# Performance work log

Measured on AMD Instinct MI355X. Metric: run time of the kernel, lower is better.

The kernel has to match this reference:

```python
import jax, jax.numpy as jnp
import numpy as np

B, N, DIM = 16, 1024, 512
H, DH = 8, 64
INNER = H * DH            # 512
FF = 4 * DIM              # 2048
CIN = 2 * DIM             # conv inner dim = dim*expansion_factor = 1024
K = 31                    # depthwise kernel size
MAXPOS = 512
EPS = 1e-5


def layernorm(x, g, b):
    mu = jnp.mean(x, axis=-1, keepdims=True)
    var = jnp.mean(jnp.square(x - mu), axis=-1, keepdims=True)
    return (x - mu) * jax.lax.rsqrt(var + EPS) * g + b


def swish(x):
    return x * jax.nn.sigmoid(x)


def feed_forward(x, w1, b1, w2, b2):
    h = swish(x @ w1 + b1)
    return h @ w2 + b2


def setup_inputs() -> dict:
    key = jax.random.key(0)
    ks = jax.random.split(key, 16)
    s = 0.02
    w = lambda k, shape: (jax.random.normal(k, shape, jnp.float32) * s)
    inp = {
        "x": jax.random.normal(ks[0], (B, N, DIM), jnp.float32),
        # FF1
        "ff1_ln_g": jnp.ones((DIM,), jnp.float32), "ff1_ln_b": jnp.zeros((DIM,), jnp.float32),
        "ff1_w1": w(ks[1], (DIM, FF)), "ff1_b1": jnp.zeros((FF,), jnp.float32),
        "ff1_w2": w(ks[2], (FF, DIM)), "ff1_b2": jnp.zeros((DIM,), jnp.float32),
        # Attention (PreNorm)
        "attn_ln_g": jnp.ones((DIM,), jnp.float32), "attn_ln_b": jnp.zeros((DIM,), jnp.float32),
        "wq": w(ks[3], (DIM, INNER)),
        "wkv": w(ks[4], (DIM, 2 * INNER)),
        "wo": w(ks[5], (INNER, DIM)), "bo": jnp.zeros((DIM,), jnp.float32),
        "rel_emb": w(ks[6], (2 * MAXPOS + 1, DH)),
        # Conv module
        "conv_ln_g": jnp.ones((DIM,), jnp.float32), "conv_ln_b": jnp.zeros((DIM,), jnp.float32),
        "conv1_w": w(ks[7], (DIM, 2 * CIN)), "conv1_b": jnp.zeros((2 * CIN,), jnp.float32),
        "dw_w": w(ks[8], (CIN, 1, K)), "dw_b": jnp.zeros((CIN,), jnp.float32),
        "conv2_w": w(ks[9], (CIN, DIM)), "conv2_b": jnp.zeros((DIM,), jnp.float32),
        # FF2
        "ff2_ln_g": jnp.ones((DIM,), jnp.float32), "ff2_ln_b": jnp.zeros((DIM,), jnp.float32),
        "ff2_w1": w(ks[10], (DIM, FF)), "ff2_b1": jnp.zeros((FF,), jnp.float32),
        "ff2_w2": w(ks[11], (FF, DIM)), "ff2_b2": jnp.zeros((DIM,), jnp.float32),
        # post norm
        "post_ln_g": jnp.ones((DIM,), jnp.float32), "post_ln_b": jnp.zeros((DIM,), jnp.float32),
    }
    return inp


def attention(x, wq, wkv, wo, bo, rel_emb):
    b, n, _ = x.shape
    scale = DH ** -0.5
    q = (x @ wq).reshape(b, n, H, DH).transpose(0, 2, 1, 3)   # b h n d
    kv = x @ wkv
    k = kv[..., :INNER].reshape(b, n, H, DH).transpose(0, 2, 1, 3)
    v = kv[..., INNER:].reshape(b, n, H, DH).transpose(0, 2, 1, 3)
    dots = jnp.einsum("bhid,bhjd->bhij", q, k) * scale
    # relative positional bias via embedding lookup
    seq = jnp.arange(n)
    dist = jnp.clip(seq[:, None] - seq[None, :], -MAXPOS, MAXPOS) + MAXPOS  # [n, n]
    rel = jnp.take(rel_emb, dist, axis=0)                      # [n, n, d]
    pos = jnp.einsum("bhnd,njd->bhnj", q, rel) * scale
    attn = jax.nn.softmax(dots + pos, axis=-1)
    out = jnp.einsum("bhij,bhjd->bhid", attn, v)
    out = out.transpose(0, 2, 1, 3).reshape(b, n, INNER)
    return out @ wo + bo


def conv_module(x, ln_g, ln_b, conv1_w, conv1_b, dw_w, dw_b, conv2_w, conv2_b):
    h = layernorm(x, ln_g, ln_b)                               # [b, n, dim]
    h = h @ conv1_w + conv1_b                                  # pointwise conv -> [b, n, 2*CIN]
    a, g = h[..., :CIN], h[..., CIN:]
    h = a * jax.nn.sigmoid(g)                                  # GLU (channel dim)
    hc = h.transpose(0, 2, 1)                                  # [b, CIN, n]
    hc = jnp.pad(hc, ((0, 0), (0, 0), (K - 1, 0)))             # causal left pad
    hc = jax.lax.conv_general_dilated(
        hc, dw_w, window_strides=(1,), padding="VALID",
        feature_group_count=CIN, dimension_numbers=("NCH", "OIH", "NCH"),
    ) + dw_b[None, :, None]
    h = hc.transpose(0, 2, 1)                                  # [b, n, CIN]
    h = swish(h)
    return h @ conv2_w + conv2_b


def reference(x, ff1_ln_g, ff1_ln_b, ff1_w1, ff1_b1, ff1_w2, ff1_b2,
              attn_ln_g, attn_ln_b, wq, wkv, wo, bo, rel_emb,
              conv_ln_g, conv_ln_b, conv1_w, conv1_b, dw_w, dw_b, conv2_w, conv2_b,
              ff2_ln_g, ff2_ln_b, ff2_w1, ff2_b1, ff2_w2, ff2_b2,
              post_ln_g, post_ln_b):
    x = 0.5 * feed_forward(layernorm(x, ff1_ln_g, ff1_ln_b), ff1_w1, ff1_b1, ff1_w2, ff1_b2) + x
    x = attention(layernorm(x, attn_ln_g, attn_ln_b), wq, wkv, wo, bo, rel_emb) + x
    x = conv_module(x, conv_ln_g, conv_ln_b, conv1_w, conv1_b, dw_w, dw_b, conv2_w, conv2_b) + x
    x = 0.5 * feed_forward(layernorm(x, ff2_ln_g, ff2_ln_b), ff2_w1, ff2_b1, ff2_w2, ff2_b2) + x
    return layernorm(x, post_ln_g, post_ln_b)
```

## Files before the change

### kernel.cpp

```cpp
#include <hip/hip_runtime.h>


#define BN 16384

typedef unsigned short u16;
typedef __attribute__((ext_vector_type(8))) __bf16 bf16x8;
typedef __attribute__((ext_vector_type(4))) float f32x4;
typedef __attribute__((ext_vector_type(8))) unsigned short u16x8;

__device__ __forceinline__ float sigf(float x) { return 1.f / (1.f + __expf(-x)); }
__device__ __forceinline__ u16 f2bf(float f) {
  unsigned int u = __float_as_uint(f);
  u += 0x7FFF + ((u >> 16) & 1);
  return (u16)(u >> 16);
}
__device__ __forceinline__ float bf2f(u16 u) {
  return __uint_as_float(((unsigned int)u) << 16);
}
__device__ __forceinline__ void gl_lds16(const void* g, void* lds) {
  __builtin_amdgcn_global_load_lds(
      (const __attribute__((address_space(1))) unsigned int*)g,
      (__attribute__((address_space(3))) unsigned int*)lds, 16, 0, 0);
}

__global__ __launch_bounds__(256) void ln_kernel(const float* __restrict__ in,
    const float* __restrict__ g, const float* __restrict__ b,
    u16* outb, float* outf) {
  const int row = blockIdx.x;
  const int t = threadIdx.x;
  const float2 v = ((const float2*)(in + (size_t)row * 512))[t];
  float s = v.x + v.y;
  float sq = v.x * v.x + v.y * v.y;
#pragma unroll
  for (int o = 32; o > 0; o >>= 1) {
    s += __shfl_down(s, o);
    sq += __shfl_down(sq, o);
  }
  __shared__ float ss[4], ssq[4];
  if ((t & 63) == 0) { ss[t >> 6] = s; ssq[t >> 6] = sq; }
  __syncthreads();
  s = ss[0] + ss[1] + ss[2] + ss[3];
  sq = ssq[0] + ssq[1] + ssq[2] + ssq[3];
  const float mu = s * (1.f / 512.f);
  const float var = fmaxf(sq * (1.f / 512.f) - mu * mu, 0.f);
  const float rstd = rsqrtf(var + 1e-5f);
  const float2 gg = ((const float2*)g)[t];
  const float2 bb = ((const float2*)b)[t];
  float ox = (v.x - mu) * rstd * gg.x + bb.x;
  float oy = (v.y - mu) * rstd * gg.y + bb.y;
  if (outf) {
    float2 o2 = {ox, oy};
    ((float2*)(outf + (size_t)row * 512))[t] = o2;
  } else {
    ushort2 u2 = {f2bf(ox), f2bf(oy)};
    ((ushort2*)(outb + (size_t)row * 512))[t] = u2;
  }
}

__global__ __launch_bounds__(256) void wtrans(const float* __restrict__ W,
                                              u16* __restrict__ WT, int K, int N) {
  const int n0 = blockIdx.x * 32, k0 = blockIdx.y * 32;
  const int t = threadIdx.x;
  const int tx = t & 31, ty = t >> 5;
  __shared__ float T[32][33];
#pragma unroll
  for (int i = 0; i < 4; ++i)
    T[tx][ty + 8 * i] = W[(size_t)(k0 + ty + 8 * i) * N + n0 + tx];
  __syncthreads();
#pragma unroll
  for (int i = 0; i < 4; ++i)
    WT[(size_t)(n0 + ty + 8 * i) * K + k0 + tx] = f2bf(T[ty + 8 * i][tx]);
}

__global__ __launch_bounds__(256) void cvt_bf16(const float* __restrict__ in,
                                                u16* __restrict__ out, int n) {
  const int i = blockIdx.x * 256 + threadIdx.x;
  if (i < n) out[i] = f2bf(in[i]);
}

__global__ __launch_bounds__(256) void gemm_bf16(const u16* __restrict__ A,
    const u16* __restrict__ WT, const float* __restrict__ bias,
    const float* res, float* Cf, u16* Cb, u16* VTout, int K, int N, int ldc,
    float alpha, int act, int qn, int vt0) {
  __shared__ __align__(16) u16 Ast[128 * 64];
  __shared__ __align__(16) u16 Bst[128 * 64];
  const int t = threadIdx.x;
  int bx = blockIdx.x, by = blockIdx.y;
  {
    const int nx = gridDim.x;
    const int lin = bx + nx * by;
    const int xcd = lin & 7;
    const int s = lin >> 3;
    const int ny8 = gridDim.y >> 3;
    const int sy = s / nx;
    by = xcd * ny8 + sy;
    bx = s - sy * nx;
  }
  const int n0 = bx * 128;
  const int m0 = by * 128;
  const int w = t >> 6;
  const int lc = t & 15, lq = (t >> 4) & 3;
  const int wy = w >> 1, wx = w & 1;
  f32x4 acc[4][4];
#pragma unroll
  for (int i = 0; i < 4; ++i)
#pragma unroll
    for (int j = 0; j < 4; ++j)
#pragma unroll
      for (int r = 0; r < 4; ++r) acc[i][j][r] = 0.f;

  const int koff0 = (lq ^ (lc & 7)) * 8;
  const int koff1 = ((4 + lq) ^ (lc & 7)) * 8;

  for (int kt = 0; kt < K; kt += 64) {
#pragma unroll
    for (int s = 0; s < 4; ++s) {
      const int f = t + 256 * s;
      const int fr = f >> 3;
      const int fc = (f & 7) ^ (fr & 7);
      gl_lds16(&A[(size_t)(m0 + fr) * K + kt + fc * 8], &Ast[f * 8]);
      gl_lds16(&WT[(size_t)(n0 + fr) * K + kt + fc * 8], &Bst[f * 8]);
    }
    __syncthreads();
#pragma unroll
    for (int kk = 0; kk < 2; ++kk) {
      const int koff = kk ? koff1 : koff0;
      bf16x8 bfr[4];
#pragma unroll
      for (int j = 0; j < 4; ++j)
        bfr[j] = *(const bf16x8*)&Bst[(wx * 64 + j * 16 + lc) * 64 + koff];
#pragma unroll
      for (int i = 0; i < 4; ++i) {
        const bf16x8 af = *(const bf16x8*)&Ast[(wy * 64 + i * 16 + lc) * 64 + koff];
#pragma unroll
        for (int j = 0; j < 4; ++j)
          acc[i][j] = __builtin_amdgcn_mfma_f32_16x16x32_bf16(af, bfr[j], acc[i][j], 0, 0, 0);
      }
    }
    __syncthreads();
  }

#pragma unroll
  for (int j = 0; j < 4; ++j) {
    const int col = n0 + wx * 64 + j * 16 + lc;
    const float bj = bias ? bias[col] : 0.f;
    const float al = (col < qn) ? alpha : 1.f;
    const bool vtc = (VTout != nullptr) && (col >= vt0);
#pragma unroll
    for (int i = 0; i < 4; ++i) {
      const int row0 = m0 + wy * 64 + i * 16 + lq * 4;
      float v4[4];
#pragma unroll
      for (int r = 0; r < 4; ++r) {
        float v = acc[i][j][r] + bj;
        if (act) v = v * sigf(v);
        v *= al;
        if (res) v += res[(size_t)(row0 + r) * ldc + col];
        v4[r] = v;
      }
      if (vtc) {
        const int cm = col - vt0;
        const int hh = cm >> 6, dd = cm & 63;
        const int bb = row0 >> 10, nl = row0 & 1023;
        ushort4 o4 = {f2bf(v4[0]), f2bf(v4[1]), f2bf(v4[2]), f2bf(v4[3])};
        *(ushort4*)&VTout[((size_t)((bb * 8 + hh) * 64 + dd)) * 1024 + nl] = o4;
      } else {
#pragma unroll
        for (int r = 0; r < 4; ++r) {
          const size_t off = (size_t)(row0 + r) * ldc + col;
          if (Cf) Cf[off] = v4[r];
          else Cb[off] = f2bf(v4[r]);
        }
      }
    }
  }
}

__global__ __launch_bounds__(256) void attn_mfma(const u16* __restrict__ QKV,
    const u16* __restrict__ Vt, const u16* __restrict__ Rb, u16* __restrict__ O) {
  const int lin = blockIdx.x;
  const int hb = lin & 127;
  const int n0 = (lin >> 7) * 64;
  const int h = hb & 7, b = hb >> 3;
  const int t = threadIdx.x;
  const int w = t >> 6;
  const int lc = t & 15, lq = (t >> 4) & 3;

  __shared__ __align__(16) u16 Ks[2][64 * 64];
  __shared__ __align__(16) u16 Vs[2][64 * 64];
  __shared__ __align__(16) u16 SP[64 * 72];

  bf16x8 qf[2];
  {
    const size_t qrow = (size_t)(b * 1024 + n0 + w * 16 + lc) * 1536 + h * 64;
    qf[0] = *(const bf16x8*)&QKV[qrow + lq * 8];
    qf[1] = *(const bf16x8*)&QKV[qrow + 32 + lq * 8];
  }

  const u16* Kg = QKV + (size_t)b * 1024 * 1536 + 512 + h * 64;
  const u16* Vg = Vt + (size_t)(b * 8 + h) * 64 * 1024;

  const int srow = t >> 3;
  const int scb0 = ((t & 7) ^ (srow & 7)) * 8;
  const int srow1 = (t + 256) >> 3;
  const int scb1 = (((t + 256) & 7) ^ (srow1 & 7)) * 8;

  gl_lds16(&Kg[(size_t)srow * 1536 + scb0], &Ks[0][t * 8]);
  gl_lds16(&Vg[(size_t)srow * 1024 + scb0], &Vs[0][t * 8]);
  gl_lds16(&Kg[(size_t)srow1 * 1536 + scb1], &Ks[0][(t + 256) * 8]);
  gl_lds16(&Vg[(size_t)srow1 * 1024 + scb1], &Vs[0][(t + 256) * 8]);

  float l_r[4] = {0.f, 0.f, 0.f, 0.f};
  f32x4 o[4];
#pragma unroll
  for (int dt = 0; dt < 4; ++dt)
#pragma unroll
    for (int r = 0; r < 4; ++r) o[dt][r] = 0.f;

  const int swz0 = (lq ^ (lc & 7)) * 8;
  const int swz1 = ((4 + lq) ^ (lc & 7)) * 8;

  int buf = 0;
  for (int jt = 0; jt < 16; ++jt) {
    const int j0 = jt * 64;
    __syncthreads();

    if (jt < 15) {
      const int j1 = j0 + 64;
      gl_lds16(&Kg[(size_t)(j1 + srow) * 1536 + scb0], &Ks[buf ^ 1][t * 8]);
      gl_lds16(&Vg[(size_t)srow * 1024 + j1 + scb0], &Vs[buf ^ 1][t * 8]);
      gl_lds16(&Kg[(size_t)(j1 + srow1) * 1536 + scb1], &Ks[buf ^ 1][(t + 256) * 8]);
      gl_lds16(&Vg[(size_t)srow1 * 1024 + j1 + scb1], &Vs[buf ^ 1][(t + 256) * 8]);
    }

    f32x4 qk[4], pa[5];
#pragma unroll
    for (int j = 0; j < 4; ++j)
#pragma unroll
      for (int r = 0; r < 4; ++r) qk[j][r] = 0.f;
#pragma unroll
    for (int rtl = 0; rtl < 5; ++rtl)
#pragma unroll
      for (int r = 0; r < 4; ++r) pa[rtl][r] = 0.f;

    const int base = n0 - j0 - 63;
    const u16* rp[5];
#pragma unroll
    for (int rtl = 0; rtl < 5; ++rtl) {
      int p = base + (w + rtl) * 16 + lc;
      p = (p < -512 ? -512 : (p > 512 ? 512 : p)) + 512;
      rp[rtl] = Rb + (size_t)p * 64 + lq * 8;
    }

#pragma unroll
    for (int ks = 0; ks < 2; ++ks) {
      const int koff = ks ? swz1 : swz0;
      bf16x8 rfr[5];
#pragma unroll
      for (int rtl = 0; rtl < 5; ++rtl)
        rfr[rtl] = *(const bf16x8*)&rp[rtl][ks * 32];
#pragma unroll
      for (int j = 0; j < 4; ++j) {
        const bf16x8 bf = *(const bf16x8*)&Ks[buf][(j * 16 + lc) * 64 + koff];
        qk[j] = __builtin_amdgcn_mfma_f32_16x16x32_bf16(qf[ks], bf, qk[j], 0, 0, 0);
      }
#pragma unroll
      for (int rtl = 0; rtl < 5; ++rtl)
        pa[rtl] = __builtin_amdgcn_mfma_f32_16x16x32_bf16(qf[ks], rfr[rtl], pa[rtl], 0, 0, 0);
    }

#pragma unroll
    for (int rtl = 0; rtl < 5; ++rtl) {
      const int didx = (w + rtl) * 16 + lc;
#pragma unroll
      for (int r = 0; r < 4; ++r) {
        const int qr = w * 16 + lq * 4 + r;
        const int jc = qr - didx + 63;
        if ((unsigned)jc < 64u) SP[qr * 72 + jc] = f2bf(pa[rtl][r]);
      }
    }

#pragma unroll
    for (int r = 0; r < 4; ++r) {
      const int qr = w * 16 + lq * 4 + r;
#pragma unroll
      for (int ti = 0; ti < 4; ++ti) {
        const int a = qr * 72 + ti * 16 + lc;
        const float e = exp2f(qk[ti][r] + bf2f(SP[a]));
        SP[a] = f2bf(e);
        l_r[r] += e;
      }
    }

#pragma unroll
    for (int ks = 0; ks < 2; ++ks) {
      const bf16x8 af = *(const bf16x8*)&SP[(w * 16 + lc) * 72 + ks * 32 + lq * 8];
      const int koff = ks ? swz1 : swz0;
#pragma unroll
      for (int dt = 0; dt < 4; ++dt) {
        const bf16x8 bf = *(const bf16x8*)&Vs[buf][(dt * 16 + lc) * 64 + koff];
        o[dt] = __builtin_amdgcn_mfma_f32_16x16x32_bf16(af, bf, o[dt], 0, 0, 0);
      }
    }
    buf ^= 1;
  }

#pragma unroll
  for (int r = 0; r < 4; ++r) {
#pragma unroll
    for (int msk = 1; msk < 16; msk <<= 1) l_r[r] += __shfl_xor(l_r[r], msk);
  }

#pragma unroll
  for (int r = 0; r < 4; ++r) {
    const float inv = 1.f / l_r[r];
    const size_t row = (size_t)(b * 1024 + n0 + w * 16 + lq * 4 + r);
#pragma unroll
    for (int dt = 0; dt < 4; ++dt)
      O[row * 512 + h * 64 + dt * 16 + lc] = f2bf(o[dt][r] * inv);
  }
}

__global__ __launch_bounds__(256) void glu_kernel(const u16* __restrict__ in,
                                                  u16* __restrict__ out) {
  const size_t m = blockIdx.x;
  const int c4 = threadIdx.x * 4;
  const ushort4 a4 = *(const ushort4*)&in[m * 2048 + c4];
  const ushort4 g4 = *(const ushort4*)&in[m * 2048 + 1024 + c4];
  ushort4 o4;
  o4.x = f2bf(bf2f(a4.x) * sigf(bf2f(g4.x)));
  o4.y = f2bf(bf2f(a4.y) * sigf(bf2f(g4.y)));
  o4.z = f2bf(bf2f(a4.z) * sigf(bf2f(g4.z)));
  o4.w = f2bf(bf2f(a4.w) * sigf(bf2f(g4.w)));
  *(ushort4*)&out[m * 1024 + c4] = o4;
}

__global__ __launch_bounds__(256) void dwconv_kernel(const u16* __restrict__ in,
    const float* __restrict__ w, const float* __restrict__ bias,
    u16* __restrict__ out) {
  const int n0 = blockIdx.x * 64;
  const int c0 = blockIdx.y * 64;
  const int b = blockIdx.z;
  const int t = threadIdx.x;
  __shared__ float hs[94][64];
  __shared__ float wsh[31][64];
  const int c = t & 63;
  const int g = t >> 6;
  for (int r = g; r < 94; r += 4) {
    const int n = n0 - 30 + r;
    hs[r][c] = (n >= 0) ? bf2f(in[(size_t)(b * 1024 + n) * 1024 + c0 + c]) : 0.f;
  }
  for (int idx = t; idx < 31 * 64; idx += 256) {
    const int tap = idx >> 6, cc = idx & 63;
    wsh[tap][cc] = w[(size_t)(c0 + cc) * 31 + tap];
  }
  __syncthreads();
  float wr[31];
#pragma unroll
  for (int k = 0; k < 31; ++k) wr[k] = wsh[k][c];
  const float bsv = bias[c0 + c];
  float win[46];
  const int rbase = g * 16;
#pragma unroll
  for (int k = 0; k < 46; ++k) win[k] = hs[rbase + k][c];
#pragma unroll
  for (int i = 0; i < 16; ++i) {
    float acc = bsv;
#pragma unroll
    for (int k = 0; k < 31; ++k) acc += wr[k] * win[i + k];
    acc = acc * sigf(acc);
    out[(size_t)(b * 1024 + n0 + rbase + i) * 1024 + c0 + c] = f2bf(acc);
  }
}

extern "C" void kernel_launch(void* const* d_in, const int* in_sizes, int n_in,
                              void* d_out, int out_size, void* d_ws, size_t ws_size,
                              hipStream_t stream) {
  const float* x        = (const float*)d_in[0];
  const float* ff1_ln_g = (const float*)d_in[1];
  const float* ff1_ln_b = (const float*)d_in[2];
  const float* ff1_w1   = (const float*)d_in[3];
  const float* ff1_b1   = (const float*)d_in[4];
  const float* ff1_w2   = (const float*)d_in[5];
  const float* ff1_b2   = (const float*)d_in[6];
  const float* attn_ln_g= (const float*)d_in[7];
  const float* attn_ln_b= (const float*)d_in[8];
  const float* wq       = (const float*)d_in[9];
  const float* wkv      = (const float*)d_in[10];
  const float* wo       = (const float*)d_in[11];
  const float* bo       = (const float*)d_in[12];
  const float* rel_emb  = (const float*)d_in[13];
  const float* conv_ln_g= (const float*)d_in[14];
  const float* conv_ln_b= (const float*)d_in[15];
  const float* conv1_w  = (const float*)d_in[16];
  const float* conv1_b  = (const float*)d_in[17];
  const float* dw_w     = (const float*)d_in[18];
  const float* dw_b     = (const float*)d_in[19];
  const float* conv2_w  = (const float*)d_in[20];
  const float* conv2_b  = (const float*)d_in[21];
  const float* ff2_ln_g = (const float*)d_in[22];
  const float* ff2_ln_b = (const float*)d_in[23];
  const float* ff2_w1   = (const float*)d_in[24];
  const float* ff2_b1   = (const float*)d_in[25];
  const float* ff2_w2   = (const float*)d_in[26];
  const float* ff2_b2   = (const float*)d_in[27];
  const float* post_ln_g= (const float*)d_in[28];
  const float* post_ln_b= (const float*)d_in[29];

  float* XRES = (float*)d_out;
  u16* ws = (u16*)d_ws;
  u16* LNB  = ws;
  u16* HID  = LNB + (size_t)BN * 512;
  u16* QKVB = HID + (size_t)BN * 2048;
  u16* VT   = QKVB + (size_t)BN * 1536;
  u16* GLUB = QKVB;
  u16* DWB  = HID;
  u16* WTp = VT + (size_t)8192 * 1024;
  u16* wt_ff1w1 = WTp;                 WTp += (size_t)2048 * 512;
  u16* wt_ff1w2 = WTp;                 WTp += (size_t)512 * 2048;
  u16* wt_qkv   = WTp;                 WTp += (size_t)1536 * 512;
  u16* wt_wo    = WTp;                 WTp += (size_t)512 * 512;
  u16* wt_conv1 = WTp;                 WTp += (size_t)2048 * 512;
  u16* wt_conv2 = WTp;                 WTp += (size_t)512 * 1024;
  u16* wt_ff2w1 = WTp;                 WTp += (size_t)2048 * 512;
  u16* wt_ff2w2 = WTp;                 WTp += (size_t)512 * 2048;
  u16* RELB     = WTp;

  const dim3 blk(256);
  const float SC = 0.125f * 1.44269504f;

  wtrans<<<dim3(64, 16), blk, 0, stream>>>(ff1_w1, wt_ff1w1, 512, 2048);
  wtrans<<<dim3(16, 64), blk, 0, stream>>>(ff1_w2, wt_ff1w2, 2048, 512);
  wtrans<<<dim3(16, 16), blk, 0, stream>>>(wq, wt_qkv, 512, 512);
  wtrans<<<dim3(32, 16), blk, 0, stream>>>(wkv, wt_qkv + (size_t)512 * 512, 512, 1024);
  wtrans<<<dim3(16, 16), blk, 0, stream>>>(wo, wt_wo, 512, 512);
  wtrans<<<dim3(64, 16), blk, 0, stream>>>(conv1_w, wt_conv1, 512, 2048);
  wtrans<<<dim3(16, 32), blk, 0, stream>>>(conv2_w, wt_conv2, 1024, 512);
  wtrans<<<dim3(64, 16), blk, 0, stream>>>(ff2_w1, wt_ff2w1, 512, 2048);
  wtrans<<<dim3(16, 64), blk, 0, stream>>>(ff2_w2, wt_ff2w2, 2048, 512);
  cvt_bf16<<<257, blk, 0, stream>>>(rel_emb, RELB, 1025 * 64);

  ln_kernel<<<BN, blk, 0, stream>>>(x, ff1_ln_g, ff1_ln_b, LNB, nullptr);
  gemm_bf16<<<dim3(16, 128), blk, 0, stream>>>(LNB, wt_ff1w1, ff1_b1, nullptr,
                                               nullptr, HID, nullptr, 512, 2048, 2048, 1.f, 1, 2048, 0);
  gemm_bf16<<<dim3(4, 128), blk, 0, stream>>>(HID, wt_ff1w2, ff1_b2, x,
                                              XRES, nullptr, nullptr, 2048, 512, 512, 0.5f, 0, 512, 0);

  ln_kernel<<<BN, blk, 0, stream>>>(XRES, attn_ln_g, attn_ln_b, LNB, nullptr);
  gemm_bf16<<<dim3(12, 128), blk, 0, stream>>>(LNB, wt_qkv, nullptr, nullptr,
                                               nullptr, QKVB, VT, 512, 1536, 1536, SC, 0, 512, 1024);
  attn_mfma<<<dim3(2048), blk, 0, stream>>>(QKVB, VT, RELB, LNB);
  gemm_bf16<<<dim3(4, 128), blk, 0, stream>>>(LNB, wt_wo, bo, XRES,
                                              XRES, nullptr, nullptr, 512, 512, 512, 1.f, 0, 512, 0);

  ln_kernel<<<BN, blk, 0, stream>>>(XRES, conv_ln_g, conv_ln_b, LNB, nullptr);
  gemm_bf16<<<dim3(16, 128), blk, 0, stream>>>(LNB, wt_conv1, conv1_b, nullptr,
                                               nullptr, HID, nullptr, 512, 2048, 2048, 1.f, 0, 2048, 0);
  glu_kernel<<<BN, blk, 0, stream>>>(HID, GLUB);
  dwconv_kernel<<<dim3(16, 16, 16), blk, 0, stream>>>(GLUB, dw_w, dw_b, DWB);
  gemm_bf16<<<dim3(4, 128), blk, 0, stream>>>(DWB, wt_conv2, conv2_b, XRES,
                                              XRES, nullptr, nullptr, 1024, 512, 512, 1.f, 0, 512, 0);

  ln_kernel<<<BN, blk, 0, stream>>>(XRES, ff2_ln_g, ff2_ln_b, LNB, nullptr);
  gemm_bf16<<<dim3(16, 128), blk, 0, stream>>>(LNB, wt_ff2w1, ff2_b1, nullptr,
                                               nullptr, HID, nullptr, 512, 2048, 2048, 1.f, 1, 2048, 0);
  gemm_bf16<<<dim3(4, 128), blk, 0, stream>>>(HID, wt_ff2w2, ff2_b2, XRES,
                                              XRES, nullptr, nullptr, 2048, 512, 512, 0.5f, 0, 512, 0);

  ln_kernel<<<BN, blk, 0, stream>>>(XRES, post_ln_g, post_ln_b, nullptr, XRES);
}
```

Before: 920.8 us.

## Double-buffer GEMM K-tiles and XOR-swizzle attention score LDS buffer

```diff
diff --git a/kernel.cpp b/kernel.cpp
--- a/kernel.cpp
+++ b/kernel.cpp
@@ -82,8 +82,8 @@
     const u16* __restrict__ WT, const float* __restrict__ bias,
     const float* res, float* Cf, u16* Cb, u16* VTout, int K, int N, int ldc,
     float alpha, int act, int qn, int vt0) {
-  __shared__ __align__(16) u16 Ast[128 * 64];
-  __shared__ __align__(16) u16 Bst[128 * 64];
+  __shared__ __align__(16) u16 Ast[2][128 * 32];
+  __shared__ __align__(16) u16 Bst[2][128 * 32];
   const int t = threadIdx.x;
   int bx = blockIdx.x, by = blockIdx.y;
   {
@@ -109,35 +109,39 @@
 #pragma unroll
       for (int r = 0; r < 4; ++r) acc[i][j][r] = 0.f;
 
-  const int koff0 = (lq ^ (lc & 7)) * 8;
-  const int koff1 = ((4 + lq) ^ (lc & 7)) * 8;
-
-  for (int kt = 0; kt < K; kt += 64) {
-#pragma unroll
-    for (int s = 0; s < 4; ++s) {
-      const int f = t + 256 * s;
-      const int fr = f >> 3;
-      const int fc = (f & 7) ^ (fr & 7);
-      gl_lds16(&A[(size_t)(m0 + fr) * K + kt + fc * 8], &Ast[f * 8]);
-      gl_lds16(&WT[(size_t)(n0 + fr) * K + kt + fc * 8], &Bst[f * 8]);
-    }
+  const int fr0 = t >> 2, fc0 = ((t & 3) ^ (fr0 & 3)) * 8;
+  const int fr1 = (t + 256) >> 2, fc1 = (((t + 256) & 3) ^ (fr1 & 3)) * 8;
+  const int koff = (lq ^ (lc & 3)) * 8;
+
+  gl_lds16(&A[(size_t)(m0 + fr0) * K + fc0], &Ast[0][t * 8]);
+  gl_lds16(&WT[(size_t)(n0 + fr0) * K + fc0], &Bst[0][t * 8]);
+  gl_lds16(&A[(size_t)(m0 + fr1) * K + fc1], &Ast[0][(t + 256) * 8]);
+  gl_lds16(&WT[(size_t)(n0 + fr1) * K + fc1], &Bst[0][(t + 256) * 8]);
+
+  int buf = 0;
+  for (int kt = 0; kt < K; kt += 32) {
     __syncthreads();
-#pragma unroll
-    for (int kk = 0; kk < 2; ++kk) {
-      const int koff = kk ? koff1 : koff0;
-      bf16x8 bfr[4];
+
+    if (kt + 32 < K) {
+      const int k2 = kt + 32;
+      gl_lds16(&A[(size_t)(m0 + fr0) * K + k2 + fc0], &Ast[buf ^ 1][t * 8]);
+      gl_lds16(&WT[(size_t)(n0 + fr0) * K + k2 + fc0], &Bst[buf ^ 1][t * 8]);
+      gl_lds16(&A[(size_t)(m0 + fr1) * K + k2 + fc1], &Ast[buf ^ 1][(t + 256) * 8]);
+      gl_lds16(&WT[(size_t)(n0 + fr1) * K + k2 + fc1], &Bst[buf ^ 1][(t + 256) * 8]);
+    }
+
+    bf16x8 bfr[4];
+#pragma unroll
+    for (int j = 0; j < 4; ++j)
+      bfr[j] = *(const bf16x8*)&Bst[buf][(wx * 64 + j * 16 + lc) * 32 + koff];
+#pragma unroll
+    for (int i = 0; i < 4; ++i) {
+      const bf16x8 af = *(const bf16x8*)&Ast[buf][(wy * 64 + i * 16 + lc) * 32 + koff];
 #pragma unroll
       for (int j = 0; j < 4; ++j)
-        bfr[j] = *(const bf16x8*)&Bst[(wx * 64 + j * 16 + lc) * 64 + koff];
-#pragma unroll
-      for (int i = 0; i < 4; ++i) {
-        const bf16x8 af = *(const bf16x8*)&Ast[(wy * 64 + i * 16 + lc) * 64 + koff];
-#pragma unroll
-        for (int j = 0; j < 4; ++j)
-          acc[i][j] = __builtin_amdgcn_mfma_f32_16x16x32_bf16(af, bfr[j], acc[i][j], 0, 0, 0);
-      }
-    }
-    __syncthreads();
+        acc[i][j] = __builtin_amdgcn_mfma_f32_16x16x32_bf16(af, bfr[j], acc[i][j], 0, 0, 0);
+    }
+    buf ^= 1;
   }
 
 #pragma unroll
@@ -188,7 +192,7 @@
 
   __shared__ __align__(16) u16 Ks[2][64 * 64];
   __shared__ __align__(16) u16 Vs[2][64 * 64];
-  __shared__ __align__(16) u16 SP[64 * 72];
+  __shared__ __align__(16) u16 SP[64 * 64];
 
   bf16x8 qf[2];
   {
@@ -276,7 +280,8 @@
       for (int r = 0; r < 4; ++r) {
         const int qr = w * 16 + lq * 4 + r;
         const int jc = qr - didx + 63;
-        if ((unsigned)jc < 64u) SP[qr * 72 + jc] = f2bf(pa[rtl][r]);
+        if ((unsigned)jc < 64u)
+          SP[qr * 64 + ((((jc >> 3) ^ (qr & 7)) << 3) | (jc & 7))] = f2bf(pa[rtl][r]);
       }
     }
 
@@ -285,7 +290,7 @@
       const int qr = w * 16 + lq * 4 + r;
 #pragma unroll
       for (int ti = 0; ti < 4; ++ti) {
-        const int a = qr * 72 + ti * 16 + lc;
+        const int a = qr * 64 + ((((ti * 2 + (lc >> 3)) ^ (qr & 7)) << 3) | (lc & 7));
         const float e = exp2f(qk[ti][r] + bf2f(SP[a]));
         SP[a] = f2bf(e);
         l_r[r] += e;
@@ -294,8 +299,8 @@
 
 #pragma unroll
     for (int ks = 0; ks < 2; ++ks) {
-      const bf16x8 af = *(const bf16x8*)&SP[(w * 16 + lc) * 72 + ks * 32 + lq * 8];
       const int koff = ks ? swz1 : swz0;
+      const bf16x8 af = *(const bf16x8*)&SP[(w * 16 + lc) * 64 + koff];
 #pragma unroll
       for (int dt = 0; dt < 4; ++dt) {
         const bf16x8 bf = *(const bf16x8*)&Vs[buf][(dt * 16 + lc) * 64 + koff];
```

After: 971.5 us. 1.06x slower.
